# Kernel optimization log

Measured on AMD Instinct MI355X. Metric: run time of the kernel, lower is better.

Reference implementation:

```python
import jax, jax.numpy as jnp
import numpy as np

B, S = 1, 2048
D = 2048            # n_embd
H = 16              # num heads
KV = 4              # num kv heads
GROUPS = H // KV
D_NOPE = 128
D_ROPE = 64
D_QK = D_NOPE + D_ROPE   # 192
D_V = 128
Q_RANK = 1536
KV_RANK = 512
EPS = 1e-6
MAX_POS = 4096


def rms_norm(x, w, eps=EPS):
    x32 = x.astype(jnp.float32)
    y = x32 * jax.lax.rsqrt(jnp.mean(x32 * x32, axis=-1, keepdims=True) + eps)
    return y.astype(x.dtype) * w


def rotate_half(x):
    x1, x2 = jnp.split(x, 2, axis=-1)
    return jnp.concatenate((-x2, x1), axis=-1)


def setup_inputs() -> dict:
    key = jax.random.key(0)
    ks = jax.random.split(key, 10)
    inv_freq = 1.0 / (10000.0 ** (jnp.arange(0, D_ROPE, 2, dtype=jnp.float32) / D_ROPE))
    t = jnp.arange(MAX_POS, dtype=jnp.float32)
    freqs = jnp.outer(t, inv_freq)                      # [MAX_POS, D_ROPE//2]
    emb = jnp.concatenate((freqs, freqs), axis=-1)      # [MAX_POS, D_ROPE]
    def lin(k, fan_in, fan_out):
        return jax.random.normal(k, (fan_in, fan_out), dtype=jnp.float32) * (fan_in ** -0.5)
    return {
        "hidden_states": jax.random.normal(ks[0], (B, S, D), dtype=jnp.float32),
        "cos": jnp.cos(emb)[None],                      # [1, MAX_POS, D_ROPE]
        "sin": jnp.sin(emb)[None],
        "wq_a": lin(ks[1], D, Q_RANK),
        "q_a_ln_w": jnp.ones((Q_RANK,), jnp.float32),
        "wq_b": lin(ks[2], Q_RANK, H * D_QK),
        "wkv_a": lin(ks[3], D, KV_RANK + D_ROPE),
        "kv_a_ln_w": jnp.ones((KV_RANK,), jnp.float32),
        "wkv_b": lin(ks[4], KV_RANK, KV * (D_NOPE + D_V)),
        "wo": lin(ks[5], H * D_V, D),
        "cache_position": jnp.arange(S, dtype=jnp.int64),
    }


def reference(hidden_states, cos, sin, wq_a, q_a_ln_w, wq_b, wkv_a, kv_a_ln_w,
              wkv_b, wo, cache_position):
    b, s, _ = hidden_states.shape
    # --- query low-rank path ---
    q_a = hidden_states @ wq_a                           # [B,S,Q_RANK]
    q = rms_norm(q_a, q_a_ln_w) @ wq_b                   # [B,S,H*D_QK]
    q = q.reshape(b, s, H, D_QK).transpose(0, 2, 1, 3)   # [B,H,S,D_QK]
    q_pass, q_rot = q[..., :D_NOPE], q[..., D_NOPE:]
    # --- kv low-rank path ---
    ckv = hidden_states @ wkv_a                          # [B,S,KV_RANK+D_ROPE]
    k_pass_a, k_rot_a = ckv[..., :KV_RANK], ckv[..., KV_RANK:]
    kv = rms_norm(k_pass_a, kv_a_ln_w) @ wkv_b           # [B,S,KV*(D_NOPE+D_V)]
    kv = kv.reshape(b, s, KV, D_NOPE + D_V).transpose(0, 2, 1, 3)  # [B,KV,S,*]
    k_pass, v = kv[..., :D_NOPE], kv[..., D_NOPE:]
    # --- partial RoPE ---
    c = cos[0][cache_position][None, None]               # [1,1,S,D_ROPE]
    sn = sin[0][cache_position][None, None]
    q_rot = q_rot * c + rotate_half(q_rot) * sn          # [B,H,S,D_ROPE]
    k_rot = k_rot_a[:, None]                             # [B,1,S,D_ROPE]
    k_rot = k_rot * c + rotate_half(k_rot) * sn
    k_rot = jnp.broadcast_to(k_rot, (b, KV, s, D_ROPE))
    k = jnp.concatenate((k_pass, k_rot), axis=-1)        # [B,KV,S,D_QK]
    # GQA expansion (repeat_interleave over head dim)
    k = jnp.repeat(k, GROUPS, axis=1)                    # [B,H,S,D_QK]
    v = jnp.repeat(v, GROUPS, axis=1)                    # [B,H,S,D_V]
    q_full = jnp.concatenate((q_pass, q_rot), axis=-1)   # [B,H,S,D_QK]
    # causal SDPA (default scale = 1/sqrt(D_QK), matching torch sdpa)
    scale = 1.0 / jnp.sqrt(jnp.float32(D_QK))
    scores = jnp.einsum("bhqd,bhkd->bhqk", q_full, k) * scale
    causal = jnp.tril(jnp.ones((s, s), dtype=bool))
    scores = jnp.where(causal[None, None], scores, jnp.finfo(scores.dtype).min)
    attn = jax.nn.softmax(scores, axis=-1)
    out = jnp.einsum("bhqk,bhkd->bhqd", attn, v)         # [B,H,S,D_V]
    out = out.transpose(0, 2, 1, 3).reshape(b, s, H * D_V)
    return out @ wo                                      # [B,S,D]
```

## Files before the change

kernel.cpp:

```cpp
#include <hip/hip_runtime.h>
#include <hip/hip_bf16.h>


#define S_LEN 2048
#define D_MODEL 2048
#define NH 16
#define NKV 4
#define D_QK 192
#define D_NOPE 128
#define D_ROPE 64
#define D_V 128
#define Q_RANK 1536
#define KV_RANK 512
#define CKV_PITCH 640
#define QDIM (NH * D_QK)
#define KVDIM (NKV * (D_NOPE + D_V))
#define ODIM (NH * D_V)
#define SCALE_QK 0.07216878364870322f
#define SPLIT 4

#define DT_B16 0
#define DT_F32 1
#define DT_AUTO 2

typedef __bf16 bf16x8 __attribute__((ext_vector_type(8)));
typedef float  f32x4  __attribute__((ext_vector_type(4)));
typedef unsigned short u16x8 __attribute__((ext_vector_type(8)));

typedef __attribute__((address_space(1))) const unsigned int as1_u32;
typedef __attribute__((address_space(3))) unsigned int as3_u32;

__device__ __forceinline__ void gl2lds16(const unsigned short* g, unsigned short* l) {
    __builtin_amdgcn_global_load_lds((as1_u32*)g, (as3_u32*)l, 16, 0, 0);
}

__device__ __forceinline__ float b2f(unsigned short u) {
    return __uint_as_float(((unsigned int)u) << 16);
}
__device__ __forceinline__ unsigned short f2b(float f) {
    unsigned int u = __float_as_uint(f);
    return (unsigned short)((u + 0x7fffu + ((u >> 16) & 1u)) >> 16);
}
__device__ __forceinline__ bool flag_f32(const unsigned* dt) {
    return dt[0] == 0x3F800000u;
}
__device__ __forceinline__ bool eff_f32(int mode, bool f32) {
    return mode == DT_F32 || (mode == DT_AUTO && f32);
}
__device__ __forceinline__ float ldany(const void* p, size_t i, bool f32) {
    return f32 ? ((const float*)p)[i] : b2f(((const unsigned short*)p)[i]);
}

#if __has_builtin(__builtin_amdgcn_mov_dpp)
#define ROR16F(x, n) __int_as_float(__builtin_amdgcn_mov_dpp(__float_as_int(x), 0x120 + (n), 0xf, 0xf, true))
#else
#define ROR16F(x, n) __shfl_xor((x), (n))
#endif

__global__ void __launch_bounds__(256)
cvt_bf16(const void* __restrict__ src, unsigned short* __restrict__ dst,
         int nelem, const unsigned* __restrict__ dt)
{
    const bool f32 = flag_f32(dt);
    for (int i = blockIdx.x * 256 + threadIdx.x; i < nelem; i += gridDim.x * 256)
        dst[i] = f2b(ldany(src, i, f32));
}

__global__ void __launch_bounds__(256)
transpose_w(const void* __restrict__ W, int Kdim, int Ncols,
            unsigned short* __restrict__ WT, const unsigned* __restrict__ dt)
{
    __shared__ unsigned short tile[64][65];
    const bool f32 = flag_f32(dt);
    const int k0 = blockIdx.x * 64, n0 = blockIdx.y * 64;
    const int t = threadIdx.x;

    for (int i = t; i < 4096; i += 256) {
        int r = i >> 6, c = i & 63;
        float v = (n0 + c < Ncols) ? ldany(W, (size_t)(k0 + r) * Ncols + n0 + c, f32) : 0.f;
        tile[c][r] = f2b(v);
    }
    __syncthreads();
    for (int i = t; i < 4096; i += 256) {
        int nn = i >> 6, kk = i & 63;
        WT[(size_t)(n0 + nn) * Kdim + k0 + kk] = tile[nn][kk];
    }
}

__global__ void __launch_bounds__(512)
gemm_mfma(const unsigned short* __restrict__ A, int lda,
          const unsigned short* __restrict__ BT, int ldb,
          void* __restrict__ C, int ldc, int K, int cm,
          const unsigned* __restrict__ dt,
          void* __restrict__ C2, int ldc2, int ncol1)
{
    __shared__ unsigned short smem[2][2][2][4096];

    const int t = threadIdx.x;
    const int w = t >> 6, lane = t & 63;
    const int half = w >> 2;
    const int wq = w & 3;
    const int wr = wq & 1, wc = wq >> 1;
    const int n = lane & 15, quad = lane >> 4;
    const int row0 = blockIdx.y << 7;
    int col0 = blockIdx.x << 7;
    const int e0 = t * 8;
    const int er = e0 >> 5, ec = e0 & 31;

    f32x4 acc[4][4];
#pragma unroll
    for (int i = 0; i < 4; ++i)
#pragma unroll
        for (int j = 0; j < 4; ++j) acc[i][j] = (f32x4){0.f, 0.f, 0.f, 0.f};

#define STAGE(BUF, KB)                                                         \
    do {                                                                       \
        gl2lds16(A  + (size_t)(row0 + er) * lda + (KB) + ec,                   \
                 &smem[BUF][0][0][e0]);                                        \
        gl2lds16(A  + (size_t)(row0 + er) * lda + (KB) + 32 + ec,              \
                 &smem[BUF][0][1][e0]);                                        \
        gl2lds16(BT + (size_t)(col0 + er) * ldb + (KB) + ec,                   \
                 &smem[BUF][1][0][e0]);                                        \
        gl2lds16(BT + (size_t)(col0 + er) * ldb + (KB) + 32 + ec,              \
                 &smem[BUF][1][1][e0]);                                        \
    } while (0)

    STAGE(0, 0);

    int cur = 0;
    for (int k0 = 0; k0 < K; k0 += 64) {
        __syncthreads();

        if (k0 + 64 < K) STAGE(cur ^ 1, k0 + 64);

        const unsigned short* Asub = &smem[cur][0][half][0];
        const unsigned short* Bsub = &smem[cur][1][half][0];

        bf16x8 af[4], bfr[4];
#pragma unroll
        for (int i = 0; i < 4; ++i)
            af[i] = *(const bf16x8*)&Asub[(wr * 64 + i * 16 + n) * 32 + quad * 8];
#pragma unroll
        for (int j = 0; j < 4; ++j)
            bfr[j] = *(const bf16x8*)&Bsub[(wc * 64 + j * 16 + n) * 32 + quad * 8];
#pragma unroll
        for (int i = 0; i < 4; ++i)
#pragma unroll
            for (int j = 0; j < 4; ++j)
                acc[i][j] = __builtin_amdgcn_mfma_f32_16x16x32_bf16(af[i], bfr[j], acc[i][j], 0, 0, 0);

        cur ^= 1;
    }
#undef STAGE

    __syncthreads();
    float* fsm = (float*)smem;
    if (half == 1) {
        float* dst = fsm + wq * 4096;
#pragma unroll
        for (int i = 0; i < 4; ++i)
#pragma unroll
            for (int j = 0; j < 4; ++j)
#pragma unroll
                for (int r = 0; r < 4; ++r)
                    dst[(i * 16 + quad * 4 + r) * 64 + j * 16 + n] = acc[i][j][r];
    }
    __syncthreads();
    if (half == 0) {
        const float* src = fsm + wq * 4096;
#pragma unroll
        for (int i = 0; i < 4; ++i)
#pragma unroll
            for (int j = 0; j < 4; ++j)
#pragma unroll
                for (int r = 0; r < 4; ++r)
                    acc[i][j][r] += src[(i * 16 + quad * 4 + r) * 64 + j * 16 + n];

        void* Cp = C; int ld = ldc;
        if (col0 >= ncol1) { Cp = C2; ld = ldc2; col0 -= ncol1; }

        const bool cf = eff_f32(cm, flag_f32(dt));
#pragma unroll
        for (int i = 0; i < 4; ++i)
#pragma unroll
            for (int r = 0; r < 4; ++r) {
                const int row = row0 + wr * 64 + i * 16 + quad * 4 + r;
                if (cf) {
                    float* crow = (float*)Cp + (size_t)row * ld + col0 + wc * 64 + n;
#pragma unroll
                    for (int j = 0; j < 4; ++j) crow[j * 16] = acc[i][j][r];
                } else {
                    unsigned short* crow = (unsigned short*)Cp + (size_t)row * ld + col0 + wc * 64 + n;
#pragma unroll
                    for (int j = 0; j < 4; ++j) crow[j * 16] = f2b(acc[i][j][r]);
                }
            }
    }
}

__global__ void __launch_bounds__(256)
rmsnorm_b(unsigned short* __restrict__ buf, int pitch, int ncols,
          const void* __restrict__ w, const unsigned* __restrict__ dt)
{
    const bool f32 = flag_f32(dt);
    const int row = blockIdx.x;
    const int t = threadIdx.x;
    unsigned short* x = buf + (size_t)row * pitch;

    float ss = 0.f;
    for (int i = t; i < ncols; i += 256) { float v = b2f(x[i]); ss += v * v; }
#pragma unroll
    for (int o = 32; o > 0; o >>= 1) ss += __shfl_down(ss, o);

    __shared__ float part[4];
    __shared__ float sc;
    if ((t & 63) == 0) part[t >> 6] = ss;
    __syncthreads();
    if (t == 0) {
        float tot = part[0] + part[1] + part[2] + part[3];
        sc = rsqrtf(tot / (float)ncols + 1e-6f);
    }
    __syncthreads();
    float scale = sc;
    for (int i = t; i < ncols; i += 256)
        x[i] = f2b(b2f(x[i]) * scale * ldany(w, i, f32));
}

__global__ void __launch_bounds__(256)
rope_k(unsigned short* __restrict__ q, unsigned short* __restrict__ ckvb,
       const void* __restrict__ cosb, const void* __restrict__ sinb,
       const void* __restrict__ cpos, const unsigned* __restrict__ dt)
{
    const bool f32 = flag_f32(dt);
    const int s = blockIdx.x;
    const int t = threadIdx.x;
    const long long* p64 = (const long long*)cpos;
    const int* p32 = (const int*)cpos;
    const bool is64 = (p64[1] == 1LL);
    const int pos = is64 ? (int)p64[s] : p32[s];
    const size_t cb = (size_t)pos * D_ROPE;

    for (int idx = t; idx < NH * 32; idx += 256) {
        int h = idx >> 5, i = idx & 31;
        unsigned short* base = q + (size_t)s * QDIM + h * D_QK + D_NOPE;
        float x1 = b2f(base[i]), x2 = b2f(base[i + 32]);
        float c1 = ldany(cosb, cb + i, f32),      s1 = ldany(sinb, cb + i, f32);
        float c2 = ldany(cosb, cb + i + 32, f32), s2 = ldany(sinb, cb + i + 32, f32);
        base[i]      = f2b(x1 * c1 - x2 * s1);
        base[i + 32] = f2b(x2 * c2 + x1 * s2);
    }
    if (t < 32) {
        int i = t;
        unsigned short* base = ckvb + (size_t)s * CKV_PITCH + KV_RANK;
        float x1 = b2f(base[i]), x2 = b2f(base[i + 32]);
        float c1 = ldany(cosb, cb + i, f32),      s1 = ldany(sinb, cb + i, f32);
        float c2 = ldany(cosb, cb + i + 32, f32), s2 = ldany(sinb, cb + i + 32, f32);
        base[i]      = f2b(x1 * c1 - x2 * s1);
        base[i + 32] = f2b(x2 * c2 + x1 * s2);
    }
}

__global__ void __launch_bounds__(256)
transpose_v(const unsigned short* __restrict__ kvb, unsigned short* __restrict__ vt)
{
    __shared__ unsigned short tile[64][68];
    const int kb = blockIdx.x;
    const int kvh = blockIdx.y >> 1;
    const int d0 = (blockIdx.y & 1) * 64;
    const int t = threadIdx.x;

    for (int i = t; i < 64 * 16; i += 256) {
        int r = i >> 4, c4 = (i & 15) << 2;
        ushort4 v = *(const ushort4*)(kvb + (size_t)(kb * 64 + r) * KVDIM
                                      + kvh * 256 + D_NOPE + d0 + c4);
        tile[c4 + 0][r] = v.x;
        tile[c4 + 1][r] = v.y;
        tile[c4 + 2][r] = v.z;
        tile[c4 + 3][r] = v.w;
    }
    __syncthreads();
    for (int i = t; i < 64 * 16; i += 256) {
        int d = i >> 4, k4 = (i & 15) << 2;
        ushort4 v = *(const ushort4*)&tile[d][k4];
        *(ushort4*)(vt + (size_t)(kvh * 128 + d0 + d) * S_LEN + kb * 64 + k4) = v;
    }
}

__global__ void __launch_bounds__(256, 2)
attn_mfma(const unsigned short* __restrict__ q, const unsigned short* __restrict__ kvb,
          const unsigned short* __restrict__ ckvb, const unsigned short* __restrict__ vt,
          unsigned short* __restrict__ pO, float* __restrict__ pm, float* __restrict__ pl)
{
    const int h   = blockIdx.y;
    const int qtb = (int)gridDim.x - 1 - (int)blockIdx.x;
    const int sp  = blockIdx.z;
    const int kvh = h >> 2;
    const int jtmax = 2 * qtb + 1;

    __shared__ unsigned short ks[64][200];
    __shared__ unsigned short vs[128][72];
    __shared__ unsigned short ps[4][2][16][72];

    const int t = threadIdx.x;
    const int w = t >> 6, lane = t & 63;
    const int n = lane & 15, quad = lane >> 4;
    const int qrow0 = qtb * 128 + w * 16;

    bf16x8 qf[2][6];
#pragma unroll
    for (int g = 0; g < 2; ++g) {
        const unsigned short* qrow = q + (size_t)(qrow0 + g * 64 + n) * QDIM + h * D_QK;
#pragma unroll
        for (int s = 0; s < 6; ++s)
            qf[g][s] = *(const bf16x8*)(qrow + s * 32 + quad * 8);
    }

    f32x4 o[2][8];
#pragma unroll
    for (int g = 0; g < 2; ++g)
#pragma unroll
        for (int c = 0; c < 8; ++c) o[g][c] = (f32x4){0.f, 0.f, 0.f, 0.f};
    float mrow[2][4], lrow[2][4];
#pragma unroll
    for (int g = 0; g < 2; ++g)
#pragma unroll
        for (int i = 0; i < 4; ++i) { mrow[g][i] = -3e38f; lrow[g][i] = 0.f; }

    u16x8 kn[4], kr[2], vv[4];

#define PRELOAD(K0)                                                            \
    {                                                                          \
        const int k0_ = (K0);                                                  \
        _Pragma("unroll")                                                      \
        for (int i = 0; i < 4; ++i) {                                          \
            int g = i * 256 + t, r = g >> 4, c = g & 15;                       \
            kn[i] = *(const u16x8*)(kvb + (size_t)(k0_ + r) * KVDIM            \
                                    + kvh * 256 + c * 8);                      \
        }                                                                      \
        _Pragma("unroll")                                                      \
        for (int i = 0; i < 2; ++i) {                                          \
            int g = i * 256 + t, r = g >> 3, c = g & 7;                        \
            kr[i] = *(const u16x8*)(ckvb + (size_t)(k0_ + r) * CKV_PITCH       \
                                    + KV_RANK + c * 8);                        \
        }                                                                      \
        _Pragma("unroll")                                                      \
        for (int i = 0; i < 4; ++i) {                                          \
            int g = i * 256 + t, d = g >> 3, c = g & 7;                        \
            vv[i] = *(const u16x8*)(vt + (size_t)(kvh * 128 + d) * S_LEN       \
                                    + k0_ + c * 8);                            \
        }                                                                      \
    }

    if (sp <= jtmax) PRELOAD(sp << 6);

    for (int jt = sp; jt <= jtmax; jt += SPLIT) {
        __syncthreads();
#pragma unroll
        for (int i = 0; i < 4; ++i) {
            int g = i * 256 + t, r = g >> 4, c = g & 15;
            *(u16x8*)&ks[r][c * 8] = kn[i];
        }
#pragma unroll
        for (int i = 0; i < 2; ++i) {
            int g = i * 256 + t, r = g >> 3, c = g & 7;
            *(u16x8*)&ks[r][128 + c * 8] = kr[i];
        }
#pragma unroll
        for (int i = 0; i < 4; ++i) {
            int g = i * 256 + t, d = g >> 3, c = g & 7;
            *(u16x8*)&vs[d][c * 8] = vv[i];
        }
        __syncthreads();

        if (jt + SPLIT <= jtmax) PRELOAD((jt + SPLIT) << 6);

        const bool act0  = (jt <= 2 * qtb);
        const bool diag0 = (jt == 2 * qtb);
        const bool diag1 = (jt == jtmax);

        f32x4 sf[2][4];
        __builtin_amdgcn_s_setprio(1);
#pragma unroll
        for (int f = 0; f < 4; ++f) {
            f32x4 a0 = (f32x4){0.f, 0.f, 0.f, 0.f};
            f32x4 a1 = (f32x4){0.f, 0.f, 0.f, 0.f};
#pragma unroll
            for (int s = 0; s < 6; ++s) {
                bf16x8 kf = *(const bf16x8*)&ks[f * 16 + n][s * 32 + quad * 8];
                a0 = __builtin_amdgcn_mfma_f32_16x16x32_bf16(qf[0][s], kf, a0, 0, 0, 0);
                a1 = __builtin_amdgcn_mfma_f32_16x16x32_bf16(qf[1][s], kf, a1, 0, 0, 0);
            }
            sf[0][f] = a0; sf[1][f] = a1;
        }
        __builtin_amdgcn_s_setprio(0);

        const bool actg[2]  = {act0, true};
        const bool diagg[2] = {diag0, diag1};

#pragma unroll
        for (int g = 0; g < 2; ++g) {
            if (!actg[g]) continue;
            const bool dg = diagg[g];
#pragma unroll
            for (int f = 0; f < 4; ++f)
#pragma unroll
                for (int i = 0; i < 4; ++i) {
                    float v = sf[g][f][i] * SCALE_QK;
                    if (dg && (f * 16 + n > w * 16 + quad * 4 + i)) v = -3e38f;
                    sf[g][f][i] = v;
                }

            float lmax[4], fac[4], alpha[4], lsum[4];
#pragma unroll
            for (int i = 0; i < 4; ++i)
                lmax[i] = fmaxf(fmaxf(fmaxf(sf[g][0][i], sf[g][1][i]),
                                      fmaxf(sf[g][2][i], sf[g][3][i])), mrow[g][i]);
#pragma unroll
            for (int f = 0; f < 4; ++f)
#pragma unroll
                for (int i = 0; i < 4; ++i)
                    sf[g][f][i] = __expf(sf[g][f][i] - lmax[i]);
#pragma unroll
            for (int i = 0; i < 4; ++i) {
                lsum[i] = (sf[g][0][i] + sf[g][1][i]) + (sf[g][2][i] + sf[g][3][i]);
                float gm = lmax[i];
                gm = fmaxf(gm, ROR16F(gm, 8));
                gm = fmaxf(gm, ROR16F(gm, 4));
                gm = fmaxf(gm, ROR16F(gm, 2));
                gm = fmaxf(gm, ROR16F(gm, 1));
                fac[i]   = __expf(lmax[i] - gm);
                alpha[i] = __expf(mrow[g][i] - gm);
                mrow[g][i] = gm;
                float s = lsum[i] * fac[i];
                s += ROR16F(s, 8);
                s += ROR16F(s, 4);
                s += ROR16F(s, 2);
                s += ROR16F(s, 1);
                lrow[g][i] = lrow[g][i] * alpha[i] + s;
#pragma unroll
                for (int c = 0; c < 8; ++c) o[g][c][i] *= alpha[i];
            }
#pragma unroll
            for (int f = 0; f < 4; ++f)
#pragma unroll
                for (int i = 0; i < 4; ++i)
                    ps[w][g][quad * 4 + i][f * 16 + n] = f2b(sf[g][f][i] * fac[i]);
        }

        __asm__ __volatile__("s_waitcnt lgkmcnt(0)" ::: "memory");

        bf16x8 pa[2][2];
#pragma unroll
        for (int g = 0; g < 2; ++g) {
            if (actg[g]) {
                pa[g][0] = *(const bf16x8*)&ps[w][g][n][quad * 8];
                pa[g][1] = *(const bf16x8*)&ps[w][g][n][32 + quad * 8];
            } else {
                pa[g][0] = (bf16x8)(__bf16)0.f;
                pa[g][1] = (bf16x8)(__bf16)0.f;
            }
        }

        __builtin_amdgcn_s_setprio(1);
#pragma unroll
        for (int c = 0; c < 8; ++c) {
            bf16x8 v0 = *(const bf16x8*)&vs[c * 16 + n][quad * 8];
            bf16x8 v1 = *(const bf16x8*)&vs[c * 16 + n][32 + quad * 8];
            o[0][c] = __builtin_amdgcn_mfma_f32_16x16x32_bf16(pa[0][0], v0, o[0][c], 0, 0, 0);
            o[0][c] = __builtin_amdgcn_mfma_f32_16x16x32_bf16(pa[0][1], v1, o[0][c], 0, 0, 0);
            o[1][c] = __builtin_amdgcn_mfma_f32_16x16x32_bf16(pa[1][0], v0, o[1][c], 0, 0, 0);
            o[1][c] = __builtin_amdgcn_mfma_f32_16x16x32_bf16(pa[1][1], v1, o[1][c], 0, 0, 0);
        }
        __builtin_amdgcn_s_setprio(0);
    }
#undef PRELOAD

#pragma unroll
    for (int g = 0; g < 2; ++g)
#pragma unroll
        for (int i = 0; i < 4; ++i) {
            const int row = qrow0 + g * 64 + quad * 4 + i;
            const size_t slot = ((size_t)(sp * S_LEN + row) * NH + h);
            unsigned short* orow = pO + slot * 128 + n;
#pragma unroll
            for (int c = 0; c < 8; ++c)
                orow[c * 16] = f2b(o[g][c][i]);
            if (n == 0) { pm[slot] = mrow[g][i]; pl[slot] = lrow[g][i]; }
        }
}

__global__ void __launch_bounds__(256)
combine_k(const unsigned short* __restrict__ pO, const float* __restrict__ pm,
          const float* __restrict__ pl, unsigned short* __restrict__ obuf)
{
    const int row = blockIdx.x;
    const int t = threadIdx.x;
    __shared__ float wsc[NH][SPLIT];

    if (t < NH) {
        const int h = t;
        float m[SPLIT], l[SPLIT];
        float mx = -3e38f;
#pragma unroll
        for (int s = 0; s < SPLIT; ++s) {
            const size_t slot = ((size_t)(s * S_LEN + row) * NH + h);
            m[s] = pm[slot]; l[s] = pl[slot];
            mx = fmaxf(mx, m[s]);
        }
        float lsum = 0.f;
#pragma unroll
        for (int s = 0; s < SPLIT; ++s) lsum += __expf(m[s] - mx) * l[s];
        float inv = 1.f / lsum;
#pragma unroll
        for (int s = 0; s < SPLIT; ++s) wsc[h][s] = __expf(m[s] - mx) * inv;
    }
    __syncthreads();

    for (int idx = t; idx < ODIM; idx += 256) {
        const int h = idx >> 7, d = idx & 127;
        float sum = 0.f;
#pragma unroll
        for (int s = 0; s < SPLIT; ++s) {
            const size_t slot = ((size_t)(s * S_LEN + row) * NH + h);
            sum += b2f(pO[slot * 128 + d]) * wsc[h][s];
        }
        obuf[(size_t)row * ODIM + idx] = f2b(sum);
    }
}


extern "C" void kernel_launch(void* const* d_in, const int* in_sizes, int n_in,
                              void* d_out, int out_size, void* d_ws, size_t ws_size,
                              hipStream_t stream)
{
    const void* hs    = d_in[0];
    const void* cosb  = d_in[1];
    const void* sinb  = d_in[2];
    const void* wq_a  = d_in[3];
    const void* q_ln  = d_in[4];
    const void* wq_b  = d_in[5];
    const void* wkv_a = d_in[6];
    const void* kv_ln = d_in[7];
    const void* wkv_b = d_in[8];
    const void* wo    = d_in[9];
    const void* cpos  = d_in[10];
    const unsigned* dt = (const unsigned*)d_in[4];

    char* ws = (char*)d_ws;
    unsigned short* woT   = (unsigned short*)ws; ws += (size_t)D_MODEL * ODIM    * 2;
    unsigned short* ckvb  = (unsigned short*)ws; ws += (size_t)S_LEN * CKV_PITCH * 2;
    unsigned short* qbuf  = (unsigned short*)ws; ws += (size_t)S_LEN * QDIM      * 2;
    unsigned short* kvb   = (unsigned short*)ws; ws += (size_t)S_LEN * KVDIM     * 2;
    unsigned short* vtb   = (unsigned short*)ws; ws += (size_t)NKV * D_V * S_LEN * 2;
    unsigned short* obuf  = (unsigned short*)ws; ws += (size_t)S_LEN * ODIM      * 2;

    char* scratch = ws;
    unsigned short* hsb   = (unsigned short*)scratch;
    unsigned short* wqaT  = hsb   + (size_t)S_LEN * D_MODEL;
    unsigned short* wkvaT = wqaT  + (size_t)Q_RANK * D_MODEL;
    unsigned short* wqbT  = wkvaT + (size_t)CKV_PITCH * D_MODEL;
    unsigned short* wkvbT = wqbT  + (size_t)QDIM * Q_RANK;
    unsigned short* q_a   = wkvbT + (size_t)KVDIM * KV_RANK;
    unsigned short* pO    = (unsigned short*)scratch;
    float*          pm    = (float*)(pO + (size_t)SPLIT * S_LEN * NH * 128);
    float*          pl    = pm + (size_t)SPLIT * S_LEN * NH;

    cvt_bf16<<<1024, 256, 0, stream>>>(hs, hsb, S_LEN * D_MODEL, dt);
    transpose_w<<<dim3(D_MODEL / 64, Q_RANK / 64), 256, 0, stream>>>(wq_a, D_MODEL, Q_RANK, wqaT, dt);
    transpose_w<<<dim3(D_MODEL / 64, CKV_PITCH / 64), 256, 0, stream>>>(wkv_a, D_MODEL, KV_RANK + D_ROPE, wkvaT, dt);
    transpose_w<<<dim3(Q_RANK / 64, QDIM / 64), 256, 0, stream>>>(wq_b, Q_RANK, QDIM, wqbT, dt);
    transpose_w<<<dim3(KV_RANK / 64, KVDIM / 64), 256, 0, stream>>>(wkv_b, KV_RANK, KVDIM, wkvbT, dt);
    transpose_w<<<dim3(D_MODEL / 64, D_MODEL / 64), 256, 0, stream>>>(wo, ODIM, D_MODEL, woT, dt);

    gemm_mfma<<<dim3((Q_RANK + CKV_PITCH) / 128, S_LEN / 128), 512, 0, stream>>>(
        hsb, D_MODEL, wqaT, D_MODEL, q_a, Q_RANK, D_MODEL, DT_B16, dt,
        ckvb, CKV_PITCH, Q_RANK);

    rmsnorm_b<<<S_LEN, 256, 0, stream>>>(q_a, Q_RANK, Q_RANK, q_ln, dt);
    rmsnorm_b<<<S_LEN, 256, 0, stream>>>(ckvb, CKV_PITCH, KV_RANK, kv_ln, dt);

    gemm_mfma<<<dim3(QDIM / 128, S_LEN / 128), 512, 0, stream>>>(
        q_a, Q_RANK, wqbT, Q_RANK, qbuf, QDIM, Q_RANK, DT_B16, dt,
        nullptr, 0, 1 << 30);
    gemm_mfma<<<dim3(KVDIM / 128, S_LEN / 128), 512, 0, stream>>>(
        ckvb, CKV_PITCH, wkvbT, KV_RANK, kvb, KVDIM, KV_RANK, DT_B16, dt,
        nullptr, 0, 1 << 30);

    rope_k<<<S_LEN, 256, 0, stream>>>(qbuf, ckvb, cosb, sinb, cpos, dt);

    transpose_v<<<dim3(S_LEN / 64, 8), 256, 0, stream>>>(kvb, vtb);

    attn_mfma<<<dim3(S_LEN / 128, NH, SPLIT), 256, 0, stream>>>(
        qbuf, kvb, ckvb, vtb, pO, pm, pl);
    combine_k<<<S_LEN, 256, 0, stream>>>(pO, pm, pl, obuf);

    gemm_mfma<<<dim3(D_MODEL / 128, S_LEN / 128), 512, 0, stream>>>(
        obuf, ODIM, woT, D_MODEL, d_out, D_MODEL, D_MODEL, DT_AUTO, dt,
        nullptr, 0, 1 << 30);
}
```

Before: 403.7 us.

## Merge independent prep, norm, GEMM and rope/transpose launches into combined kernels

Folds the input conversion and five weight transposes into one prep kernel dispatched by block index. It also merges the two RMSNorms into one launch, the Q-up and KV-up GEMMs into one grouped GEMM launch, and rope with the V transpose into one kernel. The GEMM body moves into a shared device function. The goal is to cut launch count and the tail idle time of small grids, at the cost of branchy block dispatch.

After: 339.6 us. -15.9%, faster.

```diff
diff --git a/kernel.cpp b/kernel.cpp
--- a/kernel.cpp
+++ b/kernel.cpp
@@ -58,23 +58,36 @@
 #endif
 
 __global__ void __launch_bounds__(256)
-cvt_bf16(const void* __restrict__ src, unsigned short* __restrict__ dst,
-         int nelem, const unsigned* __restrict__ dt)
+prep_k(const void* __restrict__ hs, unsigned short* __restrict__ hsb,
+       const void* __restrict__ wq_a, unsigned short* __restrict__ wqaT,
+       const void* __restrict__ wkv_a, unsigned short* __restrict__ wkvaT,
+       const void* __restrict__ wq_b, unsigned short* __restrict__ wqbT,
+       const void* __restrict__ wkv_b, unsigned short* __restrict__ wkvbT,
+       const void* __restrict__ wo, unsigned short* __restrict__ woT,
+       const unsigned* __restrict__ dt)
 {
     const bool f32 = flag_f32(dt);
-    for (int i = blockIdx.x * 256 + threadIdx.x; i < nelem; i += gridDim.x * 256)
-        dst[i] = f2b(ldany(src, i, f32));
-}
-
-__global__ void __launch_bounds__(256)
-transpose_w(const void* __restrict__ W, int Kdim, int Ncols,
-            unsigned short* __restrict__ WT, const unsigned* __restrict__ dt)
-{
+    const int t = threadIdx.x;
+    int id = blockIdx.x;
+
+    if (id < 1024) {
+        const int base = id * 4096;
+        for (int i = t; i < 4096; i += 256)
+            hsb[base + i] = f2b(ldany(hs, base + i, f32));
+        return;
+    }
+    id -= 1024;
+
+    const void* W; unsigned short* WT; int Kdim, Ncols, nkb;
+    if (id < 768)        { W = wq_a;  WT = wqaT;  Kdim = D_MODEL; Ncols = Q_RANK;           nkb = 32; }
+    else if (id < 1088)  { id -= 768;  W = wkv_a; WT = wkvaT; Kdim = D_MODEL; Ncols = KV_RANK + D_ROPE; nkb = 32; }
+    else if (id < 2240)  { id -= 1088; W = wq_b;  WT = wqbT;  Kdim = Q_RANK;  Ncols = QDIM;  nkb = 24; }
+    else if (id < 2368)  { id -= 2240; W = wkv_b; WT = wkvbT; Kdim = KV_RANK; Ncols = KVDIM; nkb = 8;  }
+    else                 { id -= 2368; W = wo;    WT = woT;   Kdim = ODIM;    Ncols = D_MODEL; nkb = 32; }
+
+    const int k0 = (id % nkb) * 64, n0 = (id / nkb) * 64;
+
     __shared__ unsigned short tile[64][65];
-    const bool f32 = flag_f32(dt);
-    const int k0 = blockIdx.x * 64, n0 = blockIdx.y * 64;
-    const int t = threadIdx.x;
-
     for (int i = t; i < 4096; i += 256) {
         int r = i >> 6, c = i & 63;
         float v = (n0 + c < Ncols) ? ldany(W, (size_t)(k0 + r) * Ncols + n0 + c, f32) : 0.f;
@@ -84,6 +97,110 @@
     for (int i = t; i < 4096; i += 256) {
         int nn = i >> 6, kk = i & 63;
         WT[(size_t)(n0 + nn) * Kdim + k0 + kk] = tile[nn][kk];
+    }
+}
+
+#define SM(BUF, MAT, SUB) (smem + (((BUF) * 4 + (MAT) * 2 + (SUB)) * 4096))
+
+__device__ __forceinline__ void
+gemm_core(unsigned short* smem,
+          const unsigned short* __restrict__ A, int lda,
+          const unsigned short* __restrict__ BT, int ldb, int colB,
+          void* __restrict__ C, int ldc, int colC, int K, bool cf, int row0)
+{
+    const int t = threadIdx.x;
+    const int w = t >> 6, lane = t & 63;
+    const int half = w >> 2;
+    const int wq = w & 3;
+    const int wr = wq & 1, wc = wq >> 1;
+    const int n = lane & 15, quad = lane >> 4;
+    const int e0 = t * 8;
+    const int er = e0 >> 5, ec = e0 & 31;
+
+    f32x4 acc[4][4];
+#pragma unroll
+    for (int i = 0; i < 4; ++i)
+#pragma unroll
+        for (int j = 0; j < 4; ++j) acc[i][j] = (f32x4){0.f, 0.f, 0.f, 0.f};
+
+#define STAGE(BUF, KB)                                                         \
+    do {                                                                       \
+        gl2lds16(A  + (size_t)(row0 + er) * lda + (KB) + ec,                   \
+                 SM(BUF, 0, 0) + e0);                                          \
+        gl2lds16(A  + (size_t)(row0 + er) * lda + (KB) + 32 + ec,              \
+                 SM(BUF, 0, 1) + e0);                                          \
+        gl2lds16(BT + (size_t)(colB + er) * ldb + (KB) + ec,                   \
+                 SM(BUF, 1, 0) + e0);                                          \
+        gl2lds16(BT + (size_t)(colB + er) * ldb + (KB) + 32 + ec,              \
+                 SM(BUF, 1, 1) + e0);                                          \
+    } while (0)
+
+    STAGE(0, 0);
+
+    int cur = 0;
+    for (int k0 = 0; k0 < K; k0 += 64) {
+        __syncthreads();
+
+        if (k0 + 64 < K) STAGE(cur ^ 1, k0 + 64);
+
+        const unsigned short* Asub = SM(cur, 0, half);
+        const unsigned short* Bsub = SM(cur, 1, half);
+
+        bf16x8 af[4], bfr[4];
+#pragma unroll
+        for (int i = 0; i < 4; ++i)
+            af[i] = *(const bf16x8*)&Asub[(wr * 64 + i * 16 + n) * 32 + quad * 8];
+#pragma unroll
+        for (int j = 0; j < 4; ++j)
+            bfr[j] = *(const bf16x8*)&Bsub[(wc * 64 + j * 16 + n) * 32 + quad * 8];
+#pragma unroll
+        for (int i = 0; i < 4; ++i)
+#pragma unroll
+            for (int j = 0; j < 4; ++j)
+                acc[i][j] = __builtin_amdgcn_mfma_f32_16x16x32_bf16(af[i], bfr[j], acc[i][j], 0, 0, 0);
+
+        cur ^= 1;
+    }
+#undef STAGE
+
+    __syncthreads();
+    float* fsm = (float*)smem;
+    if (half == 1) {
+        float* dst = fsm + wq * 4096;
+#pragma unroll
+        for (int i = 0; i < 4; ++i)
+#pragma unroll
+            for (int j = 0; j < 4; ++j)
+#pragma unroll
+                for (int r = 0; r < 4; ++r)
+                    dst[(i * 16 + quad * 4 + r) * 64 + j * 16 + n] = acc[i][j][r];
+    }
+    __syncthreads();
+    if (half == 0) {
+        const float* src = fsm + wq * 4096;
+#pragma unroll
+        for (int i = 0; i < 4; ++i)
+#pragma unroll
+            for (int j = 0; j < 4; ++j)
+#pragma unroll
+                for (int r = 0; r < 4; ++r)
+                    acc[i][j][r] += src[(i * 16 + quad * 4 + r) * 64 + j * 16 + n];
+
+#pragma unroll
+        for (int i = 0; i < 4; ++i)
+#pragma unroll
+            for (int r = 0; r < 4; ++r) {
+                const int row = row0 + wr * 64 + i * 16 + quad * 4 + r;
+                if (cf) {
+                    float* crow = (float*)C + (size_t)row * ldc + colC + wc * 64 + n;
+#pragma unroll
+                    for (int j = 0; j < 4; ++j) crow[j * 16] = acc[i][j][r];
+                } else {
+                    unsigned short* crow = (unsigned short*)C + (size_t)row * ldc + colC + wc * 64 + n;
+#pragma unroll
+                    for (int j = 0; j < 4; ++j) crow[j * 16] = f2b(acc[i][j][r]);
+                }
+            }
     }
 }
 
@@ -94,118 +211,49 @@
           const unsigned* __restrict__ dt,
           void* __restrict__ C2, int ldc2, int ncol1)
 {
-    __shared__ unsigned short smem[2][2][2][4096];
-
-    const int t = threadIdx.x;
-    const int w = t >> 6, lane = t & 63;
-    const int half = w >> 2;
-    const int wq = w & 3;
-    const int wr = wq & 1, wc = wq >> 1;
-    const int n = lane & 15, quad = lane >> 4;
+    __shared__ unsigned short smem[2 * 2 * 2 * 4096];
     const int row0 = blockIdx.y << 7;
-    int col0 = blockIdx.x << 7;
-    const int e0 = t * 8;
-    const int er = e0 >> 5, ec = e0 & 31;
-
-    f32x4 acc[4][4];
-#pragma unroll
-    for (int i = 0; i < 4; ++i)
-#pragma unroll
-        for (int j = 0; j < 4; ++j) acc[i][j] = (f32x4){0.f, 0.f, 0.f, 0.f};
-
-#define STAGE(BUF, KB)                                                         \
-    do {                                                                       \
-        gl2lds16(A  + (size_t)(row0 + er) * lda + (KB) + ec,                   \
-                 &smem[BUF][0][0][e0]);                                        \
-        gl2lds16(A  + (size_t)(row0 + er) * lda + (KB) + 32 + ec,              \
-                 &smem[BUF][0][1][e0]);                                        \
-        gl2lds16(BT + (size_t)(col0 + er) * ldb + (KB) + ec,                   \
-                 &smem[BUF][1][0][e0]);                                        \
-        gl2lds16(BT + (size_t)(col0 + er) * ldb + (KB) + 32 + ec,              \
-                 &smem[BUF][1][1][e0]);                                        \
-    } while (0)
-
-    STAGE(0, 0);
-
-    int cur = 0;
-    for (int k0 = 0; k0 < K; k0 += 64) {
-        __syncthreads();
-
-        if (k0 + 64 < K) STAGE(cur ^ 1, k0 + 64);
-
-        const unsigned short* Asub = &smem[cur][0][half][0];
-        const unsigned short* Bsub = &smem[cur][1][half][0];
-
-        bf16x8 af[4], bfr[4];
-#pragma unroll
-        for (int i = 0; i < 4; ++i)
-            af[i] = *(const bf16x8*)&Asub[(wr * 64 + i * 16 + n) * 32 + quad * 8];
-#pragma unroll
-        for (int j = 0; j < 4; ++j)
-            bfr[j] = *(const bf16x8*)&Bsub[(wc * 64 + j * 16 + n) * 32 + quad * 8];
-#pragma unroll
-        for (int i = 0; i < 4; ++i)
-#pragma unroll
-            for (int j = 0; j < 4; ++j)
-                acc[i][j] = __builtin_amdgcn_mfma_f32_16x16x32_bf16(af[i], bfr[j], acc[i][j], 0, 0, 0);
-
-        cur ^= 1;
-    }
-#undef STAGE
-
-    __syncthreads();
-    float* fsm = (float*)smem;
-    if (half == 1) {
-        float* dst = fsm + wq * 4096;
-#pragma unroll
-        for (int i = 0; i < 4; ++i)
-#pragma unroll
-            for (int j = 0; j < 4; ++j)
-#pragma unroll
-                for (int r = 0; r < 4; ++r)
-                    dst[(i * 16 + quad * 4 + r) * 64 + j * 16 + n] = acc[i][j][r];
-    }
-    __syncthreads();
-    if (half == 0) {
-        const float* src = fsm + wq * 4096;
-#pragma unroll
-        for (int i = 0; i < 4; ++i)
-#pragma unroll
-            for (int j = 0; j < 4; ++j)
-#pragma unroll
-                for (int r = 0; r < 4; ++r)
-                    acc[i][j][r] += src[(i * 16 + quad * 4 + r) * 64 + j * 16 + n];
-
-        void* Cp = C; int ld = ldc;
-        if (col0 >= ncol1) { Cp = C2; ld = ldc2; col0 -= ncol1; }
-
-        const bool cf = eff_f32(cm, flag_f32(dt));
-#pragma unroll
-        for (int i = 0; i < 4; ++i)
-#pragma unroll
-            for (int r = 0; r < 4; ++r) {
-                const int row = row0 + wr * 64 + i * 16 + quad * 4 + r;
-                if (cf) {
-                    float* crow = (float*)Cp + (size_t)row * ld + col0 + wc * 64 + n;
-#pragma unroll
-                    for (int j = 0; j < 4; ++j) crow[j * 16] = acc[i][j][r];
-                } else {
-                    unsigned short* crow = (unsigned short*)Cp + (size_t)row * ld + col0 + wc * 64 + n;
-#pragma unroll
-                    for (int j = 0; j < 4; ++j) crow[j * 16] = f2b(acc[i][j][r]);
-                }
-            }
+    const int colB = blockIdx.x << 7;
+    void* Cp = C; int ld = ldc; int colC = colB;
+    if (colC >= ncol1) { Cp = C2; ld = ldc2; colC -= ncol1; }
+    const bool cf = eff_f32(cm, flag_f32(dt));
+    gemm_core(smem, A, lda, BT, ldb, colB, Cp, ld, colC, K, cf, row0);
+}
+
+__global__ void __launch_bounds__(512)
+gemm2_mfma(const unsigned short* __restrict__ A1, int lda1,
+           const unsigned short* __restrict__ BT1, int ldb1,
+           void* __restrict__ C1, int ldc1, int K1, int nbx1, int nblk1,
+           const unsigned short* __restrict__ A2, int lda2,
+           const unsigned short* __restrict__ BT2, int ldb2,
+           void* __restrict__ C2, int ldc2, int K2, int nbx2)
+{
+    __shared__ unsigned short smem[2 * 2 * 2 * 4096];
+    int id = blockIdx.x;
+    if (id < nblk1) {
+        const int bx = id % nbx1, by = id / nbx1;
+        gemm_core(smem, A1, lda1, BT1, ldb1, bx << 7, C1, ldc1, bx << 7, K1, false, by << 7);
+    } else {
+        id -= nblk1;
+        const int bx = id % nbx2, by = id / nbx2;
+        gemm_core(smem, A2, lda2, BT2, ldb2, bx << 7, C2, ldc2, bx << 7, K2, false, by << 7);
     }
 }
 
 __global__ void __launch_bounds__(256)
-rmsnorm_b(unsigned short* __restrict__ buf, int pitch, int ncols,
-          const void* __restrict__ w, const unsigned* __restrict__ dt)
+rmsnorm2(unsigned short* __restrict__ qa, const void* __restrict__ qw,
+         unsigned short* __restrict__ ckvb, const void* __restrict__ kw,
+         const unsigned* __restrict__ dt)
 {
     const bool f32 = flag_f32(dt);
     const int row = blockIdx.x;
     const int t = threadIdx.x;
-    unsigned short* x = buf + (size_t)row * pitch;
+
+    unsigned short* x;
+    const void* w;
+    int ncols;
+    if (row < S_LEN) { x = qa + (size_t)row * Q_RANK; w = qw; ncols = Q_RANK; }
+    else             { x = ckvb + (size_t)(row - S_LEN) * CKV_PITCH; w = kw; ncols = KV_RANK; }
 
     float ss = 0.f;
     for (int i = t; i < ncols; i += 256) { float v = b2f(x[i]); ss += v * v; }
@@ -227,47 +275,51 @@
 }
 
 __global__ void __launch_bounds__(256)
-rope_k(unsigned short* __restrict__ q, unsigned short* __restrict__ ckvb,
-       const void* __restrict__ cosb, const void* __restrict__ sinb,
-       const void* __restrict__ cpos, const unsigned* __restrict__ dt)
-{
-    const bool f32 = flag_f32(dt);
-    const int s = blockIdx.x;
+rope_tv(unsigned short* __restrict__ q, unsigned short* __restrict__ ckvb,
+        const void* __restrict__ cosb, const void* __restrict__ sinb,
+        const void* __restrict__ cpos,
+        const unsigned short* __restrict__ kvb, unsigned short* __restrict__ vt,
+        const unsigned* __restrict__ dt)
+{
     const int t = threadIdx.x;
-    const long long* p64 = (const long long*)cpos;
-    const int* p32 = (const int*)cpos;
-    const bool is64 = (p64[1] == 1LL);
-    const int pos = is64 ? (int)p64[s] : p32[s];
-    const size_t cb = (size_t)pos * D_ROPE;
-
-    for (int idx = t; idx < NH * 32; idx += 256) {
-        int h = idx >> 5, i = idx & 31;
-        unsigned short* base = q + (size_t)s * QDIM + h * D_QK + D_NOPE;
-        float x1 = b2f(base[i]), x2 = b2f(base[i + 32]);
-        float c1 = ldany(cosb, cb + i, f32),      s1 = ldany(sinb, cb + i, f32);
-        float c2 = ldany(cosb, cb + i + 32, f32), s2 = ldany(sinb, cb + i + 32, f32);
-        base[i]      = f2b(x1 * c1 - x2 * s1);
-        base[i + 32] = f2b(x2 * c2 + x1 * s2);
-    }
-    if (t < 32) {
-        int i = t;
-        unsigned short* base = ckvb + (size_t)s * CKV_PITCH + KV_RANK;
-        float x1 = b2f(base[i]), x2 = b2f(base[i + 32]);
-        float c1 = ldany(cosb, cb + i, f32),      s1 = ldany(sinb, cb + i, f32);
-        float c2 = ldany(cosb, cb + i + 32, f32), s2 = ldany(sinb, cb + i + 32, f32);
-        base[i]      = f2b(x1 * c1 - x2 * s1);
-        base[i + 32] = f2b(x2 * c2 + x1 * s2);
-    }
-}
-
-__global__ void __launch_bounds__(256)
-transpose_v(const unsigned short* __restrict__ kvb, unsigned short* __restrict__ vt)
-{
+    const int bid = blockIdx.x;
+
+    if (bid < S_LEN) {
+        const bool f32 = flag_f32(dt);
+        const int s = bid;
+        const long long* p64 = (const long long*)cpos;
+        const int* p32 = (const int*)cpos;
+        const bool is64 = (p64[1] == 1LL);
+        const int pos = is64 ? (int)p64[s] : p32[s];
+        const size_t cb = (size_t)pos * D_ROPE;
+
+        for (int idx = t; idx < NH * 32; idx += 256) {
+            int h = idx >> 5, i = idx & 31;
+            unsigned short* base = q + (size_t)s * QDIM + h * D_QK + D_NOPE;
+            float x1 = b2f(base[i]), x2 = b2f(base[i + 32]);
+            float c1 = ldany(cosb, cb + i, f32),      s1 = ldany(sinb, cb + i, f32);
+            float c2 = ldany(cosb, cb + i + 32, f32), s2 = ldany(sinb, cb + i + 32, f32);
+            base[i]      = f2b(x1 * c1 - x2 * s1);
+            base[i + 32] = f2b(x2 * c2 + x1 * s2);
+        }
+        if (t < 32) {
+            int i = t;
+            unsigned short* base = ckvb + (size_t)s * CKV_PITCH + KV_RANK;
+            float x1 = b2f(base[i]), x2 = b2f(base[i + 32]);
+            float c1 = ldany(cosb, cb + i, f32),      s1 = ldany(sinb, cb + i, f32);
+            float c2 = ldany(cosb, cb + i + 32, f32), s2 = ldany(sinb, cb + i + 32, f32);
+            base[i]      = f2b(x1 * c1 - x2 * s1);
+            base[i + 32] = f2b(x2 * c2 + x1 * s2);
+        }
+        return;
+    }
+
     __shared__ unsigned short tile[64][68];
-    const int kb = blockIdx.x;
-    const int kvh = blockIdx.y >> 1;
-    const int d0 = (blockIdx.y & 1) * 64;
-    const int t = threadIdx.x;
+    const int id2 = bid - S_LEN;
+    const int kb = id2 & 31;
+    const int yy = id2 >> 5;
+    const int kvh = yy >> 1;
+    const int d0 = (yy & 1) * 64;
 
     for (int i = t; i < 64 * 16; i += 256) {
         int r = i >> 4, c4 = (i & 15) << 2;
@@ -565,33 +617,27 @@
     float*          pm    = (float*)(pO + (size_t)SPLIT * S_LEN * NH * 128);
     float*          pl    = pm + (size_t)SPLIT * S_LEN * NH;
 
-    cvt_bf16<<<1024, 256, 0, stream>>>(hs, hsb, S_LEN * D_MODEL, dt);
-    transpose_w<<<dim3(D_MODEL / 64, Q_RANK / 64), 256, 0, stream>>>(wq_a, D_MODEL, Q_RANK, wqaT, dt);
-    transpose_w<<<dim3(D_MODEL / 64, CKV_PITCH / 64), 256, 0, stream>>>(wkv_a, D_MODEL, KV_RANK + D_ROPE, wkvaT, dt);
-    transpose_w<<<dim3(Q_RANK / 64, QDIM / 64), 256, 0, stream>>>(wq_b, Q_RANK, QDIM, wqbT, dt);
-    transpose_w<<<dim3(KV_RANK / 64, KVDIM / 64), 256, 0, stream>>>(wkv_b, KV_RANK, KVDIM, wkvbT, dt);
-    transpose_w<<<dim3(D_MODEL / 64, D_MODEL / 64), 256, 0, stream>>>(wo, ODIM, D_MODEL, woT, dt);
+    prep_k<<<4416, 256, 0, stream>>>(hs, hsb, wq_a, wqaT, wkv_a, wkvaT,
+                                     wq_b, wqbT, wkv_b, wkvbT, wo, woT, dt);
 
     gemm_mfma<<<dim3((Q_RANK + CKV_PITCH) / 128, S_LEN / 128), 512, 0, stream>>>(
         hsb, D_MODEL, wqaT, D_MODEL, q_a, Q_RANK, D_MODEL, DT_B16, dt,
         ckvb, CKV_PITCH, Q_RANK);
 
-    rmsnorm_b<<<S_LEN, 256, 0, stream>>>(q_a, Q_RANK, Q_RANK, q_ln, dt);
-    rmsnorm_b<<<S_LEN, 256, 0, stream>>>(ckvb, CKV_PITCH, KV_RANK, kv_ln, dt);
-
-    gemm_mfma<<<dim3(QDIM / 128, S_LEN / 128), 512, 0, stream>>>(
-        q_a, Q_RANK, wqbT, Q_RANK, qbuf, QDIM, Q_RANK, DT_B16, dt,
-        nullptr, 0, 1 << 30);
-    gemm_mfma<<<dim3(KVDIM / 128, S_LEN / 128), 512, 0, stream>>>(
-        ckvb, CKV_PITCH, wkvbT, KV_RANK, kvb, KVDIM, KV_RANK, DT_B16, dt,
-        nullptr, 0, 1 << 30);
-
-    rope_k<<<S_LEN, 256, 0, stream>>>(qbuf, ckvb, cosb, sinb, cpos, dt);
-
-    transpose_v<<<dim3(S_LEN / 64, 8), 256, 0, stream>>>(kvb, vtb);
+    rmsnorm2<<<2 * S_LEN, 256, 0, stream>>>(q_a, q_ln, ckvb, kv_ln, dt);
+
+    gemm2_mfma<<<(QDIM / 128) * (S_LEN / 128) + (KVDIM / 128) * (S_LEN / 128),
+                 512, 0, stream>>>(
+        q_a, Q_RANK, wqbT, Q_RANK, qbuf, QDIM, Q_RANK, QDIM / 128,
+        (QDIM / 128) * (S_LEN / 128),
+        ckvb, CKV_PITCH, wkvbT, KV_RANK, kvb, KVDIM, KV_RANK, KVDIM / 128);
+
+    rope_tv<<<S_LEN + (S_LEN / 64) * 8, 256, 0, stream>>>(
+        qbuf, ckvb, cosb, sinb, cpos, kvb, vtb, dt);
 
     attn_mfma<<<dim3(S_LEN / 128, NH, SPLIT), 256, 0, stream>>>(
         qbuf, kvb, ckvb, vtb, pO, pm, pl);
+
     combine_k<<<S_LEN, 256, 0, stream>>>(pO, pm, pl, obuf);
 
     gemm_mfma<<<dim3(D_MODEL / 128, S_LEN / 128), 512, 0, stream>>>(
```
